# Kernel tuning notes

Hardware: AMD Instinct MI355X
Metric: run time of the kernel (lower is better)

The kernel has to match this reference:

```python
import jax, jax.numpy as jnp
import numpy as np

N = 100_000
E = 1_600_000
D_IN = 128
D_HID = 128
D_OUT = 16
K = 3  # PyG TAGConv default number of hops


def setup_inputs() -> dict:
    key = jax.random.key(0)
    ks = jax.random.split(key, 5)
    x = jax.random.normal(ks[0], (N, D_IN), dtype=jnp.float32)
    edge_index = jax.random.randint(ks[1], (2, E), 0, N, dtype=jnp.int32)
    # TAGConv has (K+1) bias-free linear layers + one shared bias per conv
    W1 = jax.random.normal(ks[2], (K + 1, D_IN, D_HID), dtype=jnp.float32) * 0.05
    b1 = jnp.zeros((D_HID,), dtype=jnp.float32)
    W2 = jax.random.normal(ks[3], (K + 1, D_HID, D_OUT), dtype=jnp.float32) * 0.05
    b2 = jnp.zeros((D_OUT,), dtype=jnp.float32)
    return {"x": x, "edge_index": edge_index, "W1": W1, "b1": b1, "W2": W2, "b2": b2}


def _tag_conv(x, src, dst, norm, W, b):
    # out = sum_{k=0..K} (A_norm^k x) @ W[k] + b
    out = x @ W[0]
    h = x
    for k in range(1, W.shape[0]):
        msg = h[src] * norm[:, None]                      # [E, d] gather
        h = jax.ops.segment_sum(msg, dst, num_segments=x.shape[0])  # scatter-add
        out = out + h @ W[k]
    return out + b


def reference(x, edge_index, W1, b1, W2, b2):
    src, dst = edge_index[0], edge_index[1]
    # gcn_norm without self-loops: deg over target nodes
    deg = jax.ops.segment_sum(jnp.ones((src.shape[0],), x.dtype), dst, num_segments=x.shape[0])
    dis = jnp.where(deg > 0, jax.lax.rsqrt(jnp.maximum(deg, 1.0)), 0.0).astype(x.dtype)
    norm = dis[src] * dis[dst]
    h = jax.nn.relu(_tag_conv(x, src, dst, norm, W1, b1))
    return _tag_conv(h, src, dst, norm, W2, b2)
```

## Files before the change

### kernel.cpp

```cpp
#include <hip/hip_runtime.h>

#define DF 128

typedef __attribute__((ext_vector_type(8))) short bf16x8;
typedef __attribute__((ext_vector_type(4))) float f32x4;

__device__ __forceinline__ ushort f2bf(float f) {
  uint u = __float_as_uint(f);
  u += 0x7fff + ((u >> 16) & 1);
  return (ushort)(u >> 16);
}
__device__ __forceinline__ float bfl(uint v) { return __uint_as_float(v << 16); }
__device__ __forceinline__ float bfh(uint v) { return __uint_as_float(v & 0xffff0000u); }
__device__ __forceinline__ float b2f(ushort s) { return __uint_as_float(((uint)s) << 16); }

__device__ __forceinline__ void gload16(const ushort* g, ushort* l) {
  __builtin_amdgcn_global_load_lds((const __attribute__((address_space(1))) void*)g,
                                   (__attribute__((address_space(3))) void*)l, 16, 0, 0);
}

__global__ __launch_bounds__(256) void prep_k(const float* __restrict__ x, ushort* __restrict__ xb,
                                              const float* __restrict__ W1, const float* __restrict__ W2,
                                              ushort* __restrict__ W1f, ushort* __restrict__ W2f,
                                              const int* __restrict__ dst, int e,
                                              int* __restrict__ deg_s, int* __restrict__ rank,
                                              int n, int B1) {
  int b = blockIdx.x, tid = threadIdx.x;
  if (b < B1) {
    int i = b * 256 + tid;
    if (i < n * 32) {
      float4 v = reinterpret_cast<const float4*>(x)[i];
      ushort4 s; s.x = f2bf(v.x); s.y = f2bf(v.y); s.z = f2bf(v.z); s.w = f2bf(v.w);
      reinterpret_cast<ushort4*>(xb)[i] = s;
    }
  } else if (b < B1 + 256) {
    int t = (b - B1) * 256 + tid;
    {
      int k = t >> 14, rem = t & 16383;
      int frag = rem >> 3, j = rem & 7;
      int nt = frag >> 8, ks = (frag >> 6) & 3, lane = frag & 63;
      int nn = nt * 16 + (lane & 15);
      int kk = ks * 32 + (lane >> 4) * 8 + j;
      W1f[t] = f2bf(W1[k * 16384 + kk * 128 + nn]);
    }
    if (t < 8192) {
      int frag = t >> 3, j = t & 7;
      int nt = frag >> 8, ks = (frag >> 6) & 3, lane = frag & 63;
      int kk = ks * 32 + (lane >> 4) * 8 + j;
      W2f[t] = f2bf(W2[nt * 2048 + kk * 16 + (lane & 15)]);
    }
  } else {
    int i = (b - B1 - 256) * 256 + tid;
    if (i < e) {
      int shard = (i >> 8) & 7;
      rank[i] = atomicAdd(&deg_s[(size_t)shard * n + dst[i]], 1);
    }
  }
}

__global__ void zero_k(ushort* Xb, ushort* Z3s, ushort* GBs3, ushort* F0, ushort* F1, int n) {
  int tid = threadIdx.x;
  if (tid < 128) { Xb[(size_t)n * 128 + tid] = 0; Z3s[(size_t)n * 128 + tid] = 0; }
  if (tid < 16) {
    GBs3[(size_t)n * 16 + tid] = 0;
    F0[(size_t)n * 16 + tid] = 0;
    F1[(size_t)n * 16 + tid] = 0;
  }
}

__global__ __launch_bounds__(256) void reduce_k(const int* __restrict__ deg_s, int n,
                                                int* __restrict__ deg, int* __restrict__ P,
                                                float* __restrict__ dis) {
  int i = blockIdx.x * 256 + threadIdx.x;
  if (i >= n) return;
  int run = 0;
#pragma unroll
  for (int s = 0; s < 8; s++) {
    int v = deg_s[(size_t)s * n + i];
    P[(size_t)s * n + i] = run;
    run += v;
  }
  deg[i] = run;
  dis[i] = run > 0 ? rsqrtf((float)run) : 0.f;
}

__global__ __launch_bounds__(256) void scan1_k(const int* __restrict__ deg, int n, int* __restrict__ partials) {
  __shared__ int sm[256];
  int base = blockIdx.x * 1024;
  int s = 0;
#pragma unroll
  for (int j = 0; j < 4; j++) { int idx = base + threadIdx.x * 4 + j; if (idx < n) s += deg[idx]; }
  sm[threadIdx.x] = s; __syncthreads();
  for (int off = 128; off > 0; off >>= 1) {
    if (threadIdx.x < off) sm[threadIdx.x] += sm[threadIdx.x + off];
    __syncthreads();
  }
  if (threadIdx.x == 0) partials[blockIdx.x] = sm[0];
}

__global__ void scan2_k(int* partials, int nb) {
  if (threadIdx.x == 0 && blockIdx.x == 0) {
    int run = 0;
    for (int i = 0; i < nb; i++) { int v = partials[i]; partials[i] = run; run += v; }
  }
}

__global__ __launch_bounds__(256) void scan3_k(const int* __restrict__ deg, int n, int e,
                                               const int* __restrict__ partials,
                                               int* __restrict__ rowptr) {
  __shared__ int sm[256];
  int base = blockIdx.x * 1024;
  int loc[4]; int s = 0;
#pragma unroll
  for (int j = 0; j < 4; j++) {
    int idx = base + threadIdx.x * 4 + j;
    int v = (idx < n) ? deg[idx] : 0;
    loc[j] = s; s += v;
  }
  sm[threadIdx.x] = s; __syncthreads();
  int tsum = s;
  for (int off = 1; off < 256; off <<= 1) {
    int v = (threadIdx.x >= (unsigned)off) ? sm[threadIdx.x - off] : 0;
    __syncthreads();
    sm[threadIdx.x] += v;
    __syncthreads();
  }
  int excl = sm[threadIdx.x] - tsum + partials[blockIdx.x];
#pragma unroll
  for (int j = 0; j < 4; j++) {
    int idx = base + threadIdx.x * 4 + j;
    if (idx < n) rowptr[idx] = excl + loc[j];
  }
  if (blockIdx.x == 0 && threadIdx.x == 0) rowptr[n] = e;
}

__global__ __launch_bounds__(256) void csr_fill_k(const int* __restrict__ src, const int* __restrict__ dst, int e,
                                                  const int* __restrict__ rank, const int* __restrict__ rowptr,
                                                  const int* __restrict__ P, int* __restrict__ colb, int n) {
  int i = blockIdx.x * 256 + threadIdx.x;
  if (i < e) {
    int d = dst[i];
    int shard = (i >> 8) & 7;
    int p = rowptr[d] + P[(size_t)shard * n + d] + rank[i];
    colb[p] = src[i];
  }
}

__global__ __launch_bounds__(256) void gemmZ_k(const ushort* __restrict__ Xb, const ushort* __restrict__ W1f,
                                               const float* __restrict__ dis,
                                               ushort* __restrict__ Z3s, ushort* __restrict__ Z2,
                                               ushort* __restrict__ Z1, ushort* __restrict__ Z0, int n) {
  __shared__ ushort wbuf[2][16384];
  int tid = threadIdx.x;
  int wid = tid >> 6, lane = tid & 63;
  int l15 = lane & 15, kgrp = lane >> 4;
  int m0 = blockIdx.x * 128 + wid * 32 + l15;
  int m1 = m0 + 16;
  int mc0 = m0 < n ? m0 : n - 1;
  int mc1 = m1 < n ? m1 : n - 1;
  float d0 = dis[mc0], d1 = dis[mc1];
  bf16x8 xf0[4], xf1[4];
#pragma unroll
  for (int ks = 0; ks < 4; ks++) {
    xf0[ks] = *reinterpret_cast<const bf16x8*>(Xb + (size_t)mc0 * 128 + ks * 32 + kgrp * 8);
    xf1[ks] = *reinterpret_cast<const bf16x8*>(Xb + (size_t)mc1 * 128 + ks * 32 + kgrp * 8);
  }

#define STAGE(B, K)                                                              \
  {                                                                              \
    const ushort* gsrc = W1f + (size_t)(K) * 16384;                              \
    _Pragma("unroll")                                                            \
    for (int it = 0; it < 8; it++) {                                             \
      int off = (it * 256 + wid * 64) * 8;                                       \
      gload16(gsrc + off + lane * 8, &wbuf[B][off + lane * 8]);                  \
    }                                                                            \
  }

  STAGE(0, 3)
  __syncthreads();

#pragma unroll
  for (int kk = 0; kk < 4; kk++) {
    const int k = 3 - kk;
    const int cb = kk & 1;
    if (kk < 3) STAGE(cb ^ 1, k - 1)
    f32x4 acc0[8], acc1[8];
#pragma unroll
    for (int nt = 0; nt < 8; nt++) {
      acc0[nt] = {0.f, 0.f, 0.f, 0.f};
      acc1[nt] = {0.f, 0.f, 0.f, 0.f};
    }
#pragma unroll
    for (int ks = 0; ks < 4; ks++) {
#pragma unroll
      for (int nt = 0; nt < 8; nt++) {
        bf16x8 wf = *reinterpret_cast<const bf16x8*>(&wbuf[cb][((nt * 4 + ks) * 64 + lane) * 8]);
        acc0[nt] = __builtin_amdgcn_mfma_f32_16x16x32_bf16(wf, xf0[ks], acc0[nt], 0, 0, 0);
        acc1[nt] = __builtin_amdgcn_mfma_f32_16x16x32_bf16(wf, xf1[ks], acc1[nt], 0, 0, 0);
      }
    }
    ushort* Out = (k == 3) ? Z3s : (k == 2) ? Z2 : (k == 1) ? Z1 : Z0;
    float sc0 = (k == 3) ? d0 : 1.f;
    float sc1 = (k == 3) ? d1 : 1.f;
#pragma unroll
    for (int nt = 0; nt < 8; nt++) {
      int ncol = nt * 16 + kgrp * 4;
      if (m0 < n) {
        ushort4 st; st.x = f2bf(sc0 * acc0[nt][0]); st.y = f2bf(sc0 * acc0[nt][1]);
        st.z = f2bf(sc0 * acc0[nt][2]); st.w = f2bf(sc0 * acc0[nt][3]);
        *reinterpret_cast<ushort4*>(Out + (size_t)m0 * 128 + ncol) = st;
      }
      if (m1 < n) {
        ushort4 st; st.x = f2bf(sc1 * acc1[nt][0]); st.y = f2bf(sc1 * acc1[nt][1]);
        st.z = f2bf(sc1 * acc1[nt][2]); st.w = f2bf(sc1 * acc1[nt][3]);
        *reinterpret_cast<ushort4*>(Out + (size_t)m1 * 128 + ncol) = st;
      }
    }
    __syncthreads();
  }
#undef STAGE
}

__global__ __launch_bounds__(256) void hop_k(const ushort* __restrict__ hin, const ushort* __restrict__ zk,
                                             const float* __restrict__ b1, ushort* __restrict__ hout,
                                             const int* __restrict__ rowptr, const int* __restrict__ colb,
                                             const float* __restrict__ dis, int n, int last) {
  int node = blockIdx.x * 16 + (threadIdx.x >> 4);
  int gl = threadIdx.x & 15;
  if (node >= n) return;
  int e0 = rowptr[node], e1 = rowptr[node + 1];
  float a0 = 0.f, a1 = 0.f, a2 = 0.f, a3 = 0.f, a4 = 0.f, a5 = 0.f, a6 = 0.f, a7 = 0.f;
  for (int ee = e0; ee < e1; ee += 8) {
    int c[8];
#pragma unroll
    for (int j = 0; j < 8; j++) {
      int idx = ee + j;
      c[j] = idx < e1 ? colb[idx] : n;
    }
    uint4 v[8];
#pragma unroll
    for (int j = 0; j < 8; j++)
      v[j] = *reinterpret_cast<const uint4*>(hin + (size_t)c[j] * 128 + gl * 8);
#pragma unroll
    for (int j = 0; j < 8; j++) {
      a0 += bfl(v[j].x); a1 += bfh(v[j].x);
      a2 += bfl(v[j].y); a3 += bfh(v[j].y);
      a4 += bfl(v[j].z); a5 += bfh(v[j].z);
      a6 += bfl(v[j].w); a7 += bfh(v[j].w);
    }
  }
  float d = dis[node];
  uint4 zr = *reinterpret_cast<const uint4*>(zk + (size_t)node * 128 + gl * 8);
  float t0 = fmaf(d, a0, bfl(zr.x)), t1 = fmaf(d, a1, bfh(zr.x));
  float t2 = fmaf(d, a2, bfl(zr.y)), t3 = fmaf(d, a3, bfh(zr.y));
  float t4 = fmaf(d, a4, bfl(zr.z)), t5 = fmaf(d, a5, bfh(zr.z));
  float t6 = fmaf(d, a6, bfl(zr.w)), t7 = fmaf(d, a7, bfh(zr.w));
  uint4 st;
  if (last) {
    float4 bv0 = *reinterpret_cast<const float4*>(b1 + gl * 8);
    float4 bv1 = *reinterpret_cast<const float4*>(b1 + gl * 8 + 4);
    t0 = fmaxf(t0 + bv0.x, 0.f); t1 = fmaxf(t1 + bv0.y, 0.f);
    t2 = fmaxf(t2 + bv0.z, 0.f); t3 = fmaxf(t3 + bv0.w, 0.f);
    t4 = fmaxf(t4 + bv1.x, 0.f); t5 = fmaxf(t5 + bv1.y, 0.f);
    t6 = fmaxf(t6 + bv1.z, 0.f); t7 = fmaxf(t7 + bv1.w, 0.f);
    st.x = (uint)f2bf(t0) | ((uint)f2bf(t1) << 16);
    st.y = (uint)f2bf(t2) | ((uint)f2bf(t3) << 16);
    st.z = (uint)f2bf(t4) | ((uint)f2bf(t5) << 16);
    st.w = (uint)f2bf(t6) | ((uint)f2bf(t7) << 16);
  } else {
    st.x = (uint)f2bf(d * t0) | ((uint)f2bf(d * t1) << 16);
    st.y = (uint)f2bf(d * t2) | ((uint)f2bf(d * t3) << 16);
    st.z = (uint)f2bf(d * t4) | ((uint)f2bf(d * t5) << 16);
    st.w = (uint)f2bf(d * t6) | ((uint)f2bf(d * t7) << 16);
  }
  *reinterpret_cast<uint4*>(hout + (size_t)node * 128 + gl * 8) = st;
}

__global__ __launch_bounds__(256) void gemm_last_k(const ushort* __restrict__ h1, const ushort* __restrict__ W2f,
                                                   const float* __restrict__ dis,
                                                   ushort* __restrict__ GB, ushort* __restrict__ GBs3, int n) {
  int wid = threadIdx.x >> 6, lane = threadIdx.x & 63;
  int kgrp = lane >> 4;
  int m = blockIdx.x * 64 + wid * 16 + (lane & 15);
  int mc = m < n ? m : n - 1;
  float dm = dis[mc];
  bf16x8 xf[4];
#pragma unroll
  for (int ks = 0; ks < 4; ks++)
    xf[ks] = *reinterpret_cast<const bf16x8*>(h1 + (size_t)mc * 128 + ks * 32 + kgrp * 8);
#pragma unroll
  for (int nt = 0; nt < 4; nt++) {
    f32x4 acc = {0.f, 0.f, 0.f, 0.f};
#pragma unroll
    for (int ks = 0; ks < 4; ks++) {
      bf16x8 wf = *reinterpret_cast<const bf16x8*>(W2f + (size_t)((nt * 4 + ks) * 64 + lane) * 8);
      acc = __builtin_amdgcn_mfma_f32_16x16x32_bf16(wf, xf[ks], acc, 0, 0, 0);
    }
    if (m < n) {
      int ncol = nt * 16 + kgrp * 4;
      ushort4 st; st.x = f2bf(acc[0]); st.y = f2bf(acc[1]); st.z = f2bf(acc[2]); st.w = f2bf(acc[3]);
      *reinterpret_cast<ushort4*>(GB + (size_t)m * 64 + ncol) = st;
      if (nt == 3) {
        ushort4 ss; ss.x = f2bf(dm * acc[0]); ss.y = f2bf(dm * acc[1]);
        ss.z = f2bf(dm * acc[2]); ss.w = f2bf(dm * acc[3]);
        *reinterpret_cast<ushort4*>(GBs3 + (size_t)m * 16 + kgrp * 4) = ss;
      }
    }
  }
}

__global__ __launch_bounds__(256) void spmm16_k(const ushort* __restrict__ in,
                                                const ushort* __restrict__ addraw, int addstride,
                                                const float* __restrict__ b2,
                                                float* __restrict__ outf, ushort* __restrict__ outb,
                                                const int* __restrict__ rowptr, const int* __restrict__ colb,
                                                const float* __restrict__ dis, int n) {
  int t = blockIdx.x * 256 + threadIdx.x;
  int node = t >> 3, cp = t & 7;
  if (node >= n) return;
  int e0 = rowptr[node], e1 = rowptr[node + 1];
  float a0 = 0.f, a1 = 0.f;
  for (int ee = e0; ee < e1; ee += 4) {
    int c[4];
#pragma unroll
    for (int j = 0; j < 4; j++) {
      int idx = ee + j;
      c[j] = idx < e1 ? colb[idx] : n;
    }
    uint v[4];
#pragma unroll
    for (int j = 0; j < 4; j++)
      v[j] = *reinterpret_cast<const uint*>(in + (size_t)c[j] * 16 + cp * 2);
#pragma unroll
    for (int j = 0; j < 4; j++) { a0 += bfl(v[j]); a1 += bfh(v[j]); }
  }
  float d = dis[node];
  uint av = *reinterpret_cast<const uint*>(addraw + (size_t)node * addstride + cp * 2);
  float t0 = fmaf(d, a0, b2f((ushort)(av & 0xffff)));
  float t1 = fmaf(d, a1, b2f((ushort)(av >> 16)));
  if (outf) {
    float2 st; st.x = t0 + b2[cp * 2]; st.y = t1 + b2[cp * 2 + 1];
    *reinterpret_cast<float2*>(outf + (size_t)node * 16 + cp * 2) = st;
  } else {
    uint pk = (uint)f2bf(d * t0) | ((uint)f2bf(d * t1) << 16);
    *reinterpret_cast<uint*>(outb + (size_t)node * 16 + cp * 2) = pk;
  }
}

extern "C" void kernel_launch(void* const* d_in, const int* in_sizes, int n_in,
                              void* d_out, int out_size, void* d_ws, size_t ws_size,
                              hipStream_t stream) {
  const float* x  = (const float*)d_in[0];
  const int*   ei = (const int*)d_in[1];
  const float* W1 = (const float*)d_in[2];
  const float* b1 = (const float*)d_in[3];
  const float* W2 = (const float*)d_in[4];
  const float* b2 = (const float*)d_in[5];
  float* out = (float*)d_out;

  const int n = in_sizes[0] / DF;
  const int e = in_sizes[1] / 2;
  const int* srcp = ei;
  const int* dstp = ei + e;

  char* ws = (char*)d_ws;
  size_t off = 0;
  auto alloc = [&](size_t bytes) -> void* {
    void* p = ws + off;
    off += (bytes + 255) & ~(size_t)255;
    return p;
  };
  ushort* Xb   = (ushort*)alloc((size_t)(n + 1) * 128 * 2);
  ushort* Z3s  = (ushort*)alloc((size_t)(n + 1) * 128 * 2);
  ushort* Z2   = (ushort*)alloc((size_t)n * 128 * 2);
  ushort* Z1   = (ushort*)alloc((size_t)n * 128 * 2);
  ushort* Z0   = (ushort*)alloc((size_t)n * 128 * 2);
  int*   deg_s = (int*)alloc((size_t)8 * n * 4);
  int*   P     = (int*)alloc((size_t)8 * n * 4);
  int*   deg   = (int*)alloc((size_t)n * 4);
  float* dis   = (float*)alloc((size_t)n * 4);
  int*   rowptr= (int*)alloc((size_t)(n + 1) * 4);
  int*   rank  = (int*)alloc((size_t)e * 4);
  int*   partials = (int*)alloc(1024 * 4);
  int*   colb  = (int*)alloc((size_t)e * 4);
  ushort* W1f  = (ushort*)alloc(4 * 128 * 128 * 2);
  ushort* W2f  = (ushort*)alloc(64 * 128 * 2);
  ushort* GBs3 = (ushort*)alloc((size_t)(n + 1) * 16 * 2);
  ushort* F0   = (ushort*)alloc((size_t)(n + 1) * 16 * 2);
  ushort* F1   = (ushort*)alloc((size_t)(n + 1) * 16 * 2);
  ushort* Tp = Xb;
  ushort* Up = Z3s;
  ushort* h1 = Xb;
  ushort* GB = Z0;

  hipMemsetAsync(deg_s, 0, (size_t)8 * n * 4, stream);

  int gE = (e + 255) / 256;
  int gN = (n + 255) / 256;
  int nb = (n + 1023) / 1024;
  int B1 = (n * 32 + 255) / 256;

  zero_k<<<1, 128, 0, stream>>>(Xb, Z3s, GBs3, F0, F1, n);
  prep_k<<<B1 + 256 + gE, 256, 0, stream>>>(x, Xb, W1, W2, W1f, W2f, dstp, e, deg_s, rank, n, B1);
  reduce_k<<<gN, 256, 0, stream>>>(deg_s, n, deg, P, dis);
  scan1_k<<<nb, 256, 0, stream>>>(deg, n, partials);
  scan2_k<<<1, 64, 0, stream>>>(partials, nb);
  scan3_k<<<nb, 256, 0, stream>>>(deg, n, e, partials, rowptr);
  csr_fill_k<<<gE, 256, 0, stream>>>(srcp, dstp, e, rank, rowptr, P, colb, n);

  int gGemmZ = (n + 127) / 128;
  int gGemm = (n + 63) / 64;
  int gHop  = (n + 15) / 16;
  int gS16  = (n * 8 + 255) / 256;

  gemmZ_k<<<gGemmZ, 256, 0, stream>>>(Xb, W1f, dis, Z3s, Z2, Z1, Z0, n);
  hop_k<<<gHop, 256, 0, stream>>>(Z3s, Z2, nullptr, Tp, rowptr, colb, dis, n, 0);
  hop_k<<<gHop, 256, 0, stream>>>(Tp, Z1, nullptr, Up, rowptr, colb, dis, n, 0);
  hop_k<<<gHop, 256, 0, stream>>>(Up, Z0, b1, h1, rowptr, colb, dis, n, 1);
  gemm_last_k<<<gGemm, 256, 0, stream>>>(h1, W2f, dis, GB, GBs3, n);

  spmm16_k<<<gS16, 256, 0, stream>>>(GBs3, GB + 32, 64, nullptr, nullptr, F0, rowptr, colb, dis, n);
  spmm16_k<<<gS16, 256, 0, stream>>>(F0,   GB + 16, 64, nullptr, nullptr, F1, rowptr, colb, dis, n);
  spmm16_k<<<gS16, 256, 0, stream>>>(F1,   GB + 0,  64, b2, out, nullptr, rowptr, colb, dis, n);
}
```

Before: 431.5 us.

## Split 128-wide features into 8 column slabs for cache-friendly hop gathers

Stores the hidden feature matrices as 8 slabs of 16 columns, each slab contiguous per node. Each hop kernel block then handles one slab, so the random neighbor gathers touch a 32-byte row in a 3.2MB slab that can stay in L2 rather than a full 256-byte row. The x-to-bf16 conversion is fused into the first GEMM, and that GEMM is co-launched with the degree-counting atomics. The dis scaling of Z3 moves into a separate pass co-launched with the CSR fill. The trade-off is 8x more hop blocks, each re-reading rowptr/colb, plus the W1 double buffering is dropped.

New measurement: 497.7 us. +15.4%, slower.

```diff
diff --git a/kernel.cpp b/kernel.cpp
--- a/kernel.cpp
+++ b/kernel.cpp
@@ -19,52 +19,114 @@
                                    (__attribute__((address_space(3))) void*)l, 16, 0, 0);
 }
 
-__global__ __launch_bounds__(256) void prep_k(const float* __restrict__ x, ushort* __restrict__ xb,
-                                              const float* __restrict__ W1, const float* __restrict__ W2,
-                                              ushort* __restrict__ W1f, ushort* __restrict__ W2f,
-                                              const int* __restrict__ dst, int e,
-                                              int* __restrict__ deg_s, int* __restrict__ rank,
-                                              int n, int B1) {
-  int b = blockIdx.x, tid = threadIdx.x;
-  if (b < B1) {
-    int i = b * 256 + tid;
-    if (i < n * 32) {
-      float4 v = reinterpret_cast<const float4*>(x)[i];
-      ushort4 s; s.x = f2bf(v.x); s.y = f2bf(v.y); s.z = f2bf(v.z); s.w = f2bf(v.w);
-      reinterpret_cast<ushort4*>(xb)[i] = s;
-    }
-  } else if (b < B1 + 256) {
-    int t = (b - B1) * 256 + tid;
-    {
-      int k = t >> 14, rem = t & 16383;
-      int frag = rem >> 3, j = rem & 7;
-      int nt = frag >> 8, ks = (frag >> 6) & 3, lane = frag & 63;
-      int nn = nt * 16 + (lane & 15);
-      int kk = ks * 32 + (lane >> 4) * 8 + j;
-      W1f[t] = f2bf(W1[k * 16384 + kk * 128 + nn]);
-    }
-    if (t < 8192) {
-      int frag = t >> 3, j = t & 7;
-      int nt = frag >> 8, ks = (frag >> 6) & 3, lane = frag & 63;
-      int kk = ks * 32 + (lane >> 4) * 8 + j;
-      W2f[t] = f2bf(W2[nt * 2048 + kk * 16 + (lane & 15)]);
-    }
-  } else {
-    int i = (b - B1 - 256) * 256 + tid;
-    if (i < e) {
-      int shard = (i >> 8) & 7;
-      rank[i] = atomicAdd(&deg_s[(size_t)shard * n + dst[i]], 1);
-    }
-  }
-}
-
-__global__ void zero_k(ushort* Xb, ushort* Z3s, ushort* GBs3, ushort* F0, ushort* F1, int n) {
+__global__ __launch_bounds__(256) void prepw_k(const float* __restrict__ W1, const float* __restrict__ W2,
+                                               ushort* __restrict__ W1f, ushort* __restrict__ W2f) {
+  int t = blockIdx.x * 256 + threadIdx.x;
+  {
+    int k = t >> 14, rem = t & 16383;
+    int frag = rem >> 3, j = rem & 7;
+    int nt = frag >> 8, ks = (frag >> 6) & 3, lane = frag & 63;
+    int nn = nt * 16 + (lane & 15);
+    int kk = ks * 32 + (lane >> 4) * 8 + j;
+    W1f[t] = f2bf(W1[k * 16384 + kk * 128 + nn]);
+  }
+  if (t < 8192) {
+    int frag = t >> 3, j = t & 7;
+    int nt = frag >> 8, ks = (frag >> 6) & 3, lane = frag & 63;
+    int kk = ks * 32 + (lane >> 4) * 8 + j;
+    W2f[t] = f2bf(W2[nt * 2048 + kk * 16 + (lane & 15)]);
+  }
+}
+
+__global__ void zero_k(ushort* BufA, ushort* Z3, ushort* GBs3, ushort* F0, ushort* F1, int n, int SL) {
   int tid = threadIdx.x;
-  if (tid < 128) { Xb[(size_t)n * 128 + tid] = 0; Z3s[(size_t)n * 128 + tid] = 0; }
+  if (tid < 128) {
+    int s = tid >> 4, c = tid & 15;
+    BufA[(size_t)s * SL + (size_t)n * 16 + c] = 0;
+    Z3[(size_t)s * SL + (size_t)n * 16 + c] = 0;
+  }
   if (tid < 16) {
     GBs3[(size_t)n * 16 + tid] = 0;
     F0[(size_t)n * 16 + tid] = 0;
     F1[(size_t)n * 16 + tid] = 0;
+  }
+}
+
+__global__ __launch_bounds__(256) void k1_k(const float* __restrict__ x, const ushort* __restrict__ W1f,
+                                            ushort* __restrict__ Z3, ushort* __restrict__ Z2,
+                                            ushort* __restrict__ Z1, ushort* __restrict__ Z0, int SL,
+                                            const int* __restrict__ dst, int e,
+                                            int* __restrict__ deg_s, int* __restrict__ rank,
+                                            int n, int GZ) {
+  __shared__ ushort wbuf[16384];
+  int b = blockIdx.x, tid = threadIdx.x;
+  if (b >= GZ) {
+    int i = (b - GZ) * 256 + tid;
+    if (i < e) {
+      int shard = (i >> 8) & 7;
+      rank[i] = atomicAdd(&deg_s[(size_t)shard * n + dst[i]], 1);
+    }
+    return;
+  }
+  int wid = tid >> 6, lane = tid & 63;
+  int l15 = lane & 15, kgrp = lane >> 4;
+  int m0 = b * 128 + wid * 32 + l15;
+  int m1 = m0 + 16;
+  int mc0 = m0 < n ? m0 : n - 1;
+  int mc1 = m1 < n ? m1 : n - 1;
+  bf16x8 xf0[4], xf1[4];
+#pragma unroll
+  for (int ks = 0; ks < 4; ks++) {
+    float4 a0 = *reinterpret_cast<const float4*>(x + (size_t)mc0 * 128 + ks * 32 + kgrp * 8);
+    float4 a1 = *reinterpret_cast<const float4*>(x + (size_t)mc0 * 128 + ks * 32 + kgrp * 8 + 4);
+    float4 b0 = *reinterpret_cast<const float4*>(x + (size_t)mc1 * 128 + ks * 32 + kgrp * 8);
+    float4 b1v = *reinterpret_cast<const float4*>(x + (size_t)mc1 * 128 + ks * 32 + kgrp * 8 + 4);
+    bf16x8 u, w;
+    u[0] = (short)f2bf(a0.x); u[1] = (short)f2bf(a0.y); u[2] = (short)f2bf(a0.z); u[3] = (short)f2bf(a0.w);
+    u[4] = (short)f2bf(a1.x); u[5] = (short)f2bf(a1.y); u[6] = (short)f2bf(a1.z); u[7] = (short)f2bf(a1.w);
+    w[0] = (short)f2bf(b0.x); w[1] = (short)f2bf(b0.y); w[2] = (short)f2bf(b0.z); w[3] = (short)f2bf(b0.w);
+    w[4] = (short)f2bf(b1v.x); w[5] = (short)f2bf(b1v.y); w[6] = (short)f2bf(b1v.z); w[7] = (short)f2bf(b1v.w);
+    xf0[ks] = u; xf1[ks] = w;
+  }
+#pragma unroll
+  for (int kk = 0; kk < 4; kk++) {
+    const int k = 3 - kk;
+    {
+      const ushort* gsrc = W1f + (size_t)k * 16384;
+#pragma unroll
+      for (int it = 0; it < 8; it++) {
+        int f = it * 256 + tid;
+        gload16(gsrc + (size_t)f * 8, &wbuf[f * 8]);
+      }
+    }
+    __syncthreads();
+    f32x4 acc0[8], acc1[8];
+#pragma unroll
+    for (int nt = 0; nt < 8; nt++) { acc0[nt] = {0.f,0.f,0.f,0.f}; acc1[nt] = {0.f,0.f,0.f,0.f}; }
+#pragma unroll
+    for (int ks = 0; ks < 4; ks++) {
+#pragma unroll
+      for (int nt = 0; nt < 8; nt++) {
+        bf16x8 wf = *reinterpret_cast<const bf16x8*>(&wbuf[((nt * 4 + ks) * 64 + lane) * 8]);
+        acc0[nt] = __builtin_amdgcn_mfma_f32_16x16x32_bf16(wf, xf0[ks], acc0[nt], 0, 0, 0);
+        acc1[nt] = __builtin_amdgcn_mfma_f32_16x16x32_bf16(wf, xf1[ks], acc1[nt], 0, 0, 0);
+      }
+    }
+    ushort* Out = (k == 3) ? Z3 : (k == 2) ? Z2 : (k == 1) ? Z1 : Z0;
+#pragma unroll
+    for (int nt = 0; nt < 8; nt++) {
+      if (m0 < n) {
+        ushort4 st; st.x = f2bf(acc0[nt][0]); st.y = f2bf(acc0[nt][1]);
+        st.z = f2bf(acc0[nt][2]); st.w = f2bf(acc0[nt][3]);
+        *reinterpret_cast<ushort4*>(Out + (size_t)nt * SL + (size_t)m0 * 16 + kgrp * 4) = st;
+      }
+      if (m1 < n) {
+        ushort4 st; st.x = f2bf(acc1[nt][0]); st.y = f2bf(acc1[nt][1]);
+        st.z = f2bf(acc1[nt][2]); st.w = f2bf(acc1[nt][3]);
+        *reinterpret_cast<ushort4*>(Out + (size_t)nt * SL + (size_t)m1 * 16 + kgrp * 4) = st;
+      }
+    }
+    __syncthreads();
   }
 }
 
@@ -134,100 +196,48 @@
   if (blockIdx.x == 0 && threadIdx.x == 0) rowptr[n] = e;
 }
 
-__global__ __launch_bounds__(256) void csr_fill_k(const int* __restrict__ src, const int* __restrict__ dst, int e,
-                                                  const int* __restrict__ rank, const int* __restrict__ rowptr,
-                                                  const int* __restrict__ P, int* __restrict__ colb, int n) {
-  int i = blockIdx.x * 256 + threadIdx.x;
-  if (i < e) {
-    int d = dst[i];
-    int shard = (i >> 8) & 7;
-    int p = rowptr[d] + P[(size_t)shard * n + d] + rank[i];
-    colb[p] = src[i];
-  }
-}
-
-__global__ __launch_bounds__(256) void gemmZ_k(const ushort* __restrict__ Xb, const ushort* __restrict__ W1f,
-                                               const float* __restrict__ dis,
-                                               ushort* __restrict__ Z3s, ushort* __restrict__ Z2,
-                                               ushort* __restrict__ Z1, ushort* __restrict__ Z0, int n) {
-  __shared__ ushort wbuf[2][16384];
-  int tid = threadIdx.x;
-  int wid = tid >> 6, lane = tid & 63;
-  int l15 = lane & 15, kgrp = lane >> 4;
-  int m0 = blockIdx.x * 128 + wid * 32 + l15;
-  int m1 = m0 + 16;
-  int mc0 = m0 < n ? m0 : n - 1;
-  int mc1 = m1 < n ? m1 : n - 1;
-  float d0 = dis[mc0], d1 = dis[mc1];
-  bf16x8 xf0[4], xf1[4];
-#pragma unroll
-  for (int ks = 0; ks < 4; ks++) {
-    xf0[ks] = *reinterpret_cast<const bf16x8*>(Xb + (size_t)mc0 * 128 + ks * 32 + kgrp * 8);
-    xf1[ks] = *reinterpret_cast<const bf16x8*>(Xb + (size_t)mc1 * 128 + ks * 32 + kgrp * 8);
-  }
-
-#define STAGE(B, K)                                                              \
-  {                                                                              \
-    const ushort* gsrc = W1f + (size_t)(K) * 16384;                              \
-    _Pragma("unroll")                                                            \
-    for (int it = 0; it < 8; it++) {                                             \
-      int off = (it * 256 + wid * 64) * 8;                                       \
-      gload16(gsrc + off + lane * 8, &wbuf[B][off + lane * 8]);                  \
-    }                                                                            \
-  }
-
-  STAGE(0, 3)
-  __syncthreads();
-
-#pragma unroll
-  for (int kk = 0; kk < 4; kk++) {
-    const int k = 3 - kk;
-    const int cb = kk & 1;
-    if (kk < 3) STAGE(cb ^ 1, k - 1)
-    f32x4 acc0[8], acc1[8];
-#pragma unroll
-    for (int nt = 0; nt < 8; nt++) {
-      acc0[nt] = {0.f, 0.f, 0.f, 0.f};
-      acc1[nt] = {0.f, 0.f, 0.f, 0.f};
-    }
-#pragma unroll
-    for (int ks = 0; ks < 4; ks++) {
-#pragma unroll
-      for (int nt = 0; nt < 8; nt++) {
-        bf16x8 wf = *reinterpret_cast<const bf16x8*>(&wbuf[cb][((nt * 4 + ks) * 64 + lane) * 8]);
-        acc0[nt] = __builtin_amdgcn_mfma_f32_16x16x32_bf16(wf, xf0[ks], acc0[nt], 0, 0, 0);
-        acc1[nt] = __builtin_amdgcn_mfma_f32_16x16x32_bf16(wf, xf1[ks], acc1[nt], 0, 0, 0);
-      }
-    }
-    ushort* Out = (k == 3) ? Z3s : (k == 2) ? Z2 : (k == 1) ? Z1 : Z0;
-    float sc0 = (k == 3) ? d0 : 1.f;
-    float sc1 = (k == 3) ? d1 : 1.f;
-#pragma unroll
-    for (int nt = 0; nt < 8; nt++) {
-      int ncol = nt * 16 + kgrp * 4;
-      if (m0 < n) {
-        ushort4 st; st.x = f2bf(sc0 * acc0[nt][0]); st.y = f2bf(sc0 * acc0[nt][1]);
-        st.z = f2bf(sc0 * acc0[nt][2]); st.w = f2bf(sc0 * acc0[nt][3]);
-        *reinterpret_cast<ushort4*>(Out + (size_t)m0 * 128 + ncol) = st;
-      }
-      if (m1 < n) {
-        ushort4 st; st.x = f2bf(sc1 * acc1[nt][0]); st.y = f2bf(sc1 * acc1[nt][1]);
-        st.z = f2bf(sc1 * acc1[nt][2]); st.w = f2bf(sc1 * acc1[nt][3]);
-        *reinterpret_cast<ushort4*>(Out + (size_t)m1 * 128 + ncol) = st;
-      }
-    }
-    __syncthreads();
-  }
-#undef STAGE
+__global__ __launch_bounds__(256) void k2_k(const int* __restrict__ src, const int* __restrict__ dst, int e,
+                                            const int* __restrict__ rank, const int* __restrict__ rowptr,
+                                            const int* __restrict__ P, int* __restrict__ colb,
+                                            ushort* __restrict__ Z3, const float* __restrict__ dis,
+                                            int n, int SL, int gE) {
+  int b = blockIdx.x, tid = threadIdx.x;
+  if (b < gE) {
+    int i = b * 256 + tid;
+    if (i < e) {
+      int d = dst[i];
+      int shard = (i >> 8) & 7;
+      int p = rowptr[d] + P[(size_t)shard * n + d] + rank[i];
+      colb[p] = src[i];
+    }
+  } else {
+    int b2 = b - gE;
+    int slab = b2 & 7;
+    int u = (b2 >> 3) * 256 + tid;
+    int i = u >> 1, gl = u & 1;
+    if (i < n) {
+      float d = dis[i];
+      ushort* p = Z3 + (size_t)slab * SL + (size_t)i * 16 + gl * 8;
+      uint4 v = *reinterpret_cast<const uint4*>(p);
+      uint4 o;
+      o.x = (uint)f2bf(d * bfl(v.x)) | ((uint)f2bf(d * bfh(v.x)) << 16);
+      o.y = (uint)f2bf(d * bfl(v.y)) | ((uint)f2bf(d * bfh(v.y)) << 16);
+      o.z = (uint)f2bf(d * bfl(v.z)) | ((uint)f2bf(d * bfh(v.z)) << 16);
+      o.w = (uint)f2bf(d * bfl(v.w)) | ((uint)f2bf(d * bfh(v.w)) << 16);
+      *reinterpret_cast<uint4*>(p) = o;
+    }
+  }
 }
 
 __global__ __launch_bounds__(256) void hop_k(const ushort* __restrict__ hin, const ushort* __restrict__ zk,
                                              const float* __restrict__ b1, ushort* __restrict__ hout,
                                              const int* __restrict__ rowptr, const int* __restrict__ colb,
-                                             const float* __restrict__ dis, int n, int last) {
-  int node = blockIdx.x * 16 + (threadIdx.x >> 4);
-  int gl = threadIdx.x & 15;
+                                             const float* __restrict__ dis, int n, int SL, int last) {
+  int slice = blockIdx.x & 7;
+  int node = (blockIdx.x >> 3) * 128 + (threadIdx.x >> 1);
+  int gl = threadIdx.x & 1;
   if (node >= n) return;
+  const ushort* sin = hin + (size_t)slice * SL;
   int e0 = rowptr[node], e1 = rowptr[node + 1];
   float a0 = 0.f, a1 = 0.f, a2 = 0.f, a3 = 0.f, a4 = 0.f, a5 = 0.f, a6 = 0.f, a7 = 0.f;
   for (int ee = e0; ee < e1; ee += 8) {
@@ -240,7 +250,7 @@
     uint4 v[8];
 #pragma unroll
     for (int j = 0; j < 8; j++)
-      v[j] = *reinterpret_cast<const uint4*>(hin + (size_t)c[j] * 128 + gl * 8);
+      v[j] = *reinterpret_cast<const uint4*>(sin + (size_t)c[j] * 16 + gl * 8);
 #pragma unroll
     for (int j = 0; j < 8; j++) {
       a0 += bfl(v[j].x); a1 += bfh(v[j].x);
@@ -250,15 +260,16 @@
     }
   }
   float d = dis[node];
-  uint4 zr = *reinterpret_cast<const uint4*>(zk + (size_t)node * 128 + gl * 8);
+  uint4 zr = *reinterpret_cast<const uint4*>(zk + (size_t)slice * SL + (size_t)node * 16 + gl * 8);
   float t0 = fmaf(d, a0, bfl(zr.x)), t1 = fmaf(d, a1, bfh(zr.x));
   float t2 = fmaf(d, a2, bfl(zr.y)), t3 = fmaf(d, a3, bfh(zr.y));
   float t4 = fmaf(d, a4, bfl(zr.z)), t5 = fmaf(d, a5, bfh(zr.z));
   float t6 = fmaf(d, a6, bfl(zr.w)), t7 = fmaf(d, a7, bfh(zr.w));
   uint4 st;
   if (last) {
-    float4 bv0 = *reinterpret_cast<const float4*>(b1 + gl * 8);
-    float4 bv1 = *reinterpret_cast<const float4*>(b1 + gl * 8 + 4);
+    int cb = slice * 16 + gl * 8;
+    float4 bv0 = *reinterpret_cast<const float4*>(b1 + cb);
+    float4 bv1 = *reinterpret_cast<const float4*>(b1 + cb + 4);
     t0 = fmaxf(t0 + bv0.x, 0.f); t1 = fmaxf(t1 + bv0.y, 0.f);
     t2 = fmaxf(t2 + bv0.z, 0.f); t3 = fmaxf(t3 + bv0.w, 0.f);
     t4 = fmaxf(t4 + bv1.x, 0.f); t5 = fmaxf(t5 + bv1.y, 0.f);
@@ -273,12 +284,13 @@
     st.z = (uint)f2bf(d * t4) | ((uint)f2bf(d * t5) << 16);
     st.w = (uint)f2bf(d * t6) | ((uint)f2bf(d * t7) << 16);
   }
-  *reinterpret_cast<uint4*>(hout + (size_t)node * 128 + gl * 8) = st;
+  *reinterpret_cast<uint4*>(hout + (size_t)slice * SL + (size_t)node * 16 + gl * 8) = st;
 }
 
 __global__ __launch_bounds__(256) void gemm_last_k(const ushort* __restrict__ h1, const ushort* __restrict__ W2f,
                                                    const float* __restrict__ dis,
-                                                   ushort* __restrict__ GB, ushort* __restrict__ GBs3, int n) {
+                                                   ushort* __restrict__ GB, ushort* __restrict__ GBs3,
+                                                   int n, int SL) {
   int wid = threadIdx.x >> 6, lane = threadIdx.x & 63;
   int kgrp = lane >> 4;
   int m = blockIdx.x * 64 + wid * 16 + (lane & 15);
@@ -286,8 +298,10 @@
   float dm = dis[mc];
   bf16x8 xf[4];
 #pragma unroll
-  for (int ks = 0; ks < 4; ks++)
-    xf[ks] = *reinterpret_cast<const bf16x8*>(h1 + (size_t)mc * 128 + ks * 32 + kgrp * 8);
+  for (int ks = 0; ks < 4; ks++) {
+    int slice = ks * 2 + (kgrp >> 1);
+    xf[ks] = *reinterpret_cast<const bf16x8*>(h1 + (size_t)slice * SL + (size_t)mc * 16 + (kgrp & 1) * 8);
+  }
 #pragma unroll
   for (int nt = 0; nt < 4; nt++) {
     f32x4 acc = {0.f, 0.f, 0.f, 0.f};
@@ -362,6 +376,7 @@
   const int e = in_sizes[1] / 2;
   const int* srcp = ei;
   const int* dstp = ei + e;
+  const int SL = (n + 1) * 16;
 
   char* ws = (char*)d_ws;
   size_t off = 0;
@@ -370,11 +385,11 @@
     off += (bytes + 255) & ~(size_t)255;
     return p;
   };
-  ushort* Xb   = (ushort*)alloc((size_t)(n + 1) * 128 * 2);
-  ushort* Z3s  = (ushort*)alloc((size_t)(n + 1) * 128 * 2);
-  ushort* Z2   = (ushort*)alloc((size_t)n * 128 * 2);
-  ushort* Z1   = (ushort*)alloc((size_t)n * 128 * 2);
-  ushort* Z0   = (ushort*)alloc((size_t)n * 128 * 2);
+  ushort* BufA = (ushort*)alloc((size_t)8 * SL * 2);
+  ushort* Z3   = (ushort*)alloc((size_t)8 * SL * 2);
+  ushort* Z2   = (ushort*)alloc((size_t)8 * SL * 2);
+  ushort* Z1   = (ushort*)alloc((size_t)8 * SL * 2);
+  ushort* Z0   = (ushort*)alloc((size_t)8 * SL * 2);
   int*   deg_s = (int*)alloc((size_t)8 * n * 4);
   int*   P     = (int*)alloc((size_t)8 * n * 4);
   int*   deg   = (int*)alloc((size_t)n * 4);
@@ -385,39 +400,39 @@
   int*   colb  = (int*)alloc((size_t)e * 4);
   ushort* W1f  = (ushort*)alloc(4 * 128 * 128 * 2);
   ushort* W2f  = (ushort*)alloc(64 * 128 * 2);
-  ushort* GBs3 = (ushort*)alloc((size_t)(n + 1) * 16 * 2);
-  ushort* F0   = (ushort*)alloc((size_t)(n + 1) * 16 * 2);
-  ushort* F1   = (ushort*)alloc((size_t)(n + 1) * 16 * 2);
-  ushort* Tp = Xb;
-  ushort* Up = Z3s;
-  ushort* h1 = Xb;
-  ushort* GB = Z0;
+  ushort* GBs3 = (ushort*)alloc((size_t)SL * 2);
+  ushort* F0   = (ushort*)alloc((size_t)SL * 2);
+  ushort* F1   = (ushort*)alloc((size_t)SL * 2);
+  ushort* Tp = BufA;
+  ushort* Up = Z3;
+  ushort* h1 = BufA;
+  ushort* GB = Z2;
 
   hipMemsetAsync(deg_s, 0, (size_t)8 * n * 4, stream);
 
   int gE = (e + 255) / 256;
   int gN = (n + 255) / 256;
   int nb = (n + 1023) / 1024;
-  int B1 = (n * 32 + 255) / 256;
-
-  zero_k<<<1, 128, 0, stream>>>(Xb, Z3s, GBs3, F0, F1, n);
-  prep_k<<<B1 + 256 + gE, 256, 0, stream>>>(x, Xb, W1, W2, W1f, W2f, dstp, e, deg_s, rank, n, B1);
+  int GZ = (n + 127) / 128;
+
+  zero_k<<<1, 256, 0, stream>>>(BufA, Z3, GBs3, F0, F1, n, SL);
+  prepw_k<<<256, 256, 0, stream>>>(W1, W2, W1f, W2f);
+  k1_k<<<GZ + gE, 256, 0, stream>>>(x, W1f, Z3, Z2, Z1, Z0, SL, dstp, e, deg_s, rank, n, GZ);
   reduce_k<<<gN, 256, 0, stream>>>(deg_s, n, deg, P, dis);
   scan1_k<<<nb, 256, 0, stream>>>(deg, n, partials);
   scan2_k<<<1, 64, 0, stream>>>(partials, nb);
   scan3_k<<<nb, 256, 0, stream>>>(deg, n, e, partials, rowptr);
-  csr_fill_k<<<gE, 256, 0, stream>>>(srcp, dstp, e, rank, rowptr, P, colb, n);
-
-  int gGemmZ = (n + 127) / 128;
+  int gScale = 8 * ((2 * n + 255) / 256);
+  k2_k<<<gE + gScale, 256, 0, stream>>>(srcp, dstp, e, rank, rowptr, P, colb, Z3, dis, n, SL, gE);
+
+  int gHop = 8 * ((n + 127) / 128);
   int gGemm = (n + 63) / 64;
-  int gHop  = (n + 15) / 16;
-  int gS16  = (n * 8 + 255) / 256;
-
-  gemmZ_k<<<gGemmZ, 256, 0, stream>>>(Xb, W1f, dis, Z3s, Z2, Z1, Z0, n);
-  hop_k<<<gHop, 256, 0, stream>>>(Z3s, Z2, nullptr, Tp, rowptr, colb, dis, n, 0);
-  hop_k<<<gHop, 256, 0, stream>>>(Tp, Z1, nullptr, Up, rowptr, colb, dis, n, 0);
-  hop_k<<<gHop, 256, 0, stream>>>(Up, Z0, b1, h1, rowptr, colb, dis, n, 1);
-  gemm_last_k<<<gGemm, 256, 0, stream>>>(h1, W2f, dis, GB, GBs3, n);
+  int gS16 = (n * 8 + 255) / 256;
+
+  hop_k<<<gHop, 256, 0, stream>>>(Z3, Z2, nullptr, Tp, rowptr, colb, dis, n, SL, 0);
+  hop_k<<<gHop, 256, 0, stream>>>(Tp, Z1, nullptr, Up, rowptr, colb, dis, n, SL, 0);
+  hop_k<<<gHop, 256, 0, stream>>>(Up, Z0, b1, h1, rowptr, colb, dis, n, SL, 1);
+  gemm_last_k<<<gGemm, 256, 0, stream>>>(h1, W2f, dis, GB, GBs3, n, SL);
 
   spmm16_k<<<gS16, 256, 0, stream>>>(GBs3, GB + 32, 64, nullptr, nullptr, F0, rowptr, colb, dis, n);
   spmm16_k<<<gS16, 256, 0, stream>>>(F0,   GB + 16, 64, nullptr, nullptr, F1, rowptr, colb, dis, n);
```
